# Kernel tuning notes

Measured on AMD Instinct MI355X. Metric: run time of the kernel, lower is better.

The kernel has to match this reference:

```python
import math
import jax, jax.numpy as jnp
import numpy as np

G = 128        # graphs per batch
N0 = 512       # nodes per graph
H = 256        # hidden size
E = 524288     # edges (avg degree 8), intra-graph
RATIO = 0.8


def setup_inputs() -> dict:
    key = jax.random.key(0)
    ks = jax.random.split(key, 16)
    # intra-graph edges: E//G edges per graph
    eg = jnp.arange(E, dtype=jnp.int32) // (E // G)
    src = eg * N0 + jax.random.randint(ks[0], (E,), 0, N0, dtype=jnp.int32)
    dst = eg * N0 + jax.random.randint(ks[1], (E,), 0, N0, dtype=jnp.int32)
    s = 1.0 / math.sqrt(H)
    return {
        "x": jax.random.normal(ks[2], (G * N0, H), jnp.float32),
        "edge_src": src,
        "edge_dst": dst,
        "W_in": jax.random.normal(ks[3], (H, H), jnp.float32) * s,
        "b_in": jnp.zeros((H,), jnp.float32),
        "W_h0": jax.random.normal(ks[4], (H, H), jnp.float32) * s,
        "b_h0": jnp.zeros((H,), jnp.float32),
        "W_h1": jax.random.normal(ks[5], (H, H), jnp.float32) * s,
        "b_h1": jnp.zeros((H,), jnp.float32),
        "p_in": jax.random.normal(ks[6], (H,), jnp.float32),
        "p_h0": jax.random.normal(ks[7], (H,), jnp.float32),
        "p_h1": jax.random.normal(ks[8], (H,), jnp.float32),
        "att_w": jax.random.normal(ks[9], (H,), jnp.float32) * s,
        "att_b": jnp.zeros((1,), jnp.float32),
    }


def gcn_conv(x, W, b, src, dst, emask, num_nodes):
    # PyG GCNConv: lin -> sym-normalized propagate (with self loops, weight 1) -> bias
    h = x @ W
    deg = jax.ops.segment_sum(emask, dst, num_segments=num_nodes) + 1.0  # +1 self loop
    dis = jax.lax.rsqrt(deg)
    coef = dis[src] * dis[dst] * emask                    # [E]
    agg = jax.ops.segment_sum(h[src] * coef[:, None], dst, num_segments=num_nodes)
    agg = agg + h * (dis * dis)[:, None]                  # self-loop message
    return agg + b


def topk_pool(x, p, src, dst, emask, n_cur):
    # PyG TopKPooling: score = tanh(x.p/|p|), keep top ceil(ratio*n) per graph,
    # x' = x[perm]*score[perm], edges filtered to kept nodes and remapped.
    k = int(math.ceil(RATIO * n_cur))
    score = jnp.tanh((x @ p) / jnp.linalg.norm(p))        # [G*n_cur]
    _, idx = jax.lax.top_k(score.reshape(G, n_cur), k)    # [G,k]
    perm = (idx + (jnp.arange(G, dtype=idx.dtype) * n_cur)[:, None]).reshape(-1)
    x_new = x[perm] * score[perm][:, None]                # [G*k,H]
    mapping = jnp.full((G * n_cur,), -1, jnp.int32).at[perm].set(
        jnp.arange(G * k, dtype=jnp.int32))
    ns, nd = mapping[src], mapping[dst]
    valid = (ns >= 0) & (nd >= 0) & (emask > 0)
    return (x_new, jnp.where(valid, ns, 0), jnp.where(valid, nd, 0),
            valid.astype(x.dtype), k)


def att_pool(x, att_w, att_b, k):
    # GlobalAttention: per-graph softmax gate, weighted sum
    gate = (x @ att_w + att_b[0]).reshape(G, k)
    att = jax.nn.softmax(gate, axis=1)
    return jnp.einsum('gk,gkh->gh', att, x.reshape(G, k, H))


def reference(x, edge_src, edge_dst, W_in, b_in, W_h0, b_h0, W_h1, b_h1,
              p_in, p_h0, p_h1, att_w, att_b):
    src, dst = edge_src, edge_dst
    emask = jnp.ones((E,), x.dtype)
    n_cur = N0
    h = jax.nn.relu(gcn_conv(x, W_in, b_in, src, dst, emask, G * n_cur))
    h, src, dst, emask, n_cur = topk_pool(h, p_in, src, dst, emask, n_cur)
    out = att_pool(h, att_w, att_b, n_cur)
    for (W, b, p) in ((W_h0, b_h0, p_h0), (W_h1, b_h1, p_h1)):
        h = jax.nn.relu(gcn_conv(h, W, b, src, dst, emask, G * n_cur))
        h, src, dst, emask, n_cur = topk_pool(h, p, src, dst, emask, n_cur)
        out = out + att_pool(h, att_w, att_b, n_cur)
    return out  # [G, H]
```

## Files before the change

### kernel.cpp

```cpp
#include <hip/hip_runtime.h>
#include <cmath>

#define G_ 128
#define N0_ 512
#define H_ 256
#define E_ 524288
#define NODES0 (G_*N0_)

typedef _Float16 v8h __attribute__((ext_vector_type(8)));
typedef _Float16 v4h __attribute__((ext_vector_type(4)));
typedef float v4f __attribute__((ext_vector_type(4)));

#define TSTRIDE 72
#define TILEHW (128*TSTRIDE)

__device__ __forceinline__ void async_copy16(void* lds, const void* g) {
  __builtin_amdgcn_global_load_lds(
      (const __attribute__((address_space(1))) void*)g,
      (__attribute__((address_space(3))) void*)lds, 16, 0, 0);
}

__device__ __forceinline__ float4 f4fma(float4 a, float s, float4 acc) {
  acc.x = fmaf(a.x, s, acc.x); acc.y = fmaf(a.y, s, acc.y);
  acc.z = fmaf(a.z, s, acc.z); acc.w = fmaf(a.w, s, acc.w);
  return acc;
}

__device__ __forceinline__ float block_reduce_sum(float v, volatile float* red) {
  #pragma unroll
  for (int off = 32; off > 0; off >>= 1) v += __shfl_down(v, off);
  int lane = threadIdx.x & 63, wid = threadIdx.x >> 6;
  __syncthreads();
  if (lane == 0) red[wid] = v;
  __syncthreads();
  return red[0] + red[1] + red[2] + red[3];
}

__global__ __launch_bounds__(256) void pnorm_kernel(const float* __restrict__ p0,
                                                    const float* __restrict__ p1,
                                                    const float* __restrict__ p2,
                                                    float* __restrict__ pinv) {
  __shared__ float red[4];
  const float* p = (blockIdx.x == 0) ? p0 : (blockIdx.x == 1 ? p1 : p2);
  float v = p[threadIdx.x];
  float s = block_reduce_sum(v * v, red);
  if (threadIdx.x == 0) pinv[blockIdx.x] = 1.0f / sqrtf(s);
}

__global__ void init_cum_kernel(int* __restrict__ cum, int* __restrict__ cnt, int n) {
  int v = blockIdx.x * 256 + threadIdx.x;
  if (v < n) { cum[v] = v; cnt[v] = 0; }
}

__global__ __launch_bounds__(256) void wconv_kernel(const float* __restrict__ W0,
                                                    const float* __restrict__ W1,
                                                    const float* __restrict__ W2,
                                                    _Float16* __restrict__ img) {
  int l = blockIdx.x >> 4;
  const float* W = (l == 0) ? W0 : (l == 1 ? W1 : W2);
  int bn = (blockIdx.x >> 3) & 1, kt = blockIdx.x & 7;
  int t = threadIdx.x;
  int n = t & 127, kh = t >> 7;
  int k0 = kt * 32 + kh * 16;
  _Float16* row = img + (size_t)l * 16 * TILEHW + ((size_t)(bn * 8 + kt) * 128 + n) * TSTRIDE;
  #pragma unroll
  for (int s = 0; s < 2; ++s) {
    v8h hv, lv;
    #pragma unroll
    for (int j = 0; j < 8; ++j) {
      float a = W[(size_t)(k0 + s * 8 + j) * 256 + bn * 128 + n];
      _Float16 h = (_Float16)a;
      hv[j] = h;
      lv[j] = (_Float16)(a - (float)h);
    }
    *(v8h*)&row[kh * 16 + s * 8] = hv;
    *(v8h*)&row[32 + kh * 16 + s * 8] = lv;
  }
}

__global__ __launch_bounds__(256) void gemm_f16x3_kernel(const float* __restrict__ A,
                                                         const _Float16* __restrict__ Wimg,
                                                         float* __restrict__ C) {
  __shared__ _Float16 As[TILEHW];
  __shared__ _Float16 Ws[TILEHW];
  const int tid = threadIdx.x;
  const int bm = blockIdx.x >> 1;
  const int bn = blockIdx.x & 1;
  const int lane = tid & 63, wid = tid >> 6;
  const int wm = wid >> 1, wn = wid & 1;
  const int l15 = lane & 15, kg = lane >> 4;

  v4f acc[4][4];
  #pragma unroll
  for (int i = 0; i < 4; ++i)
    #pragma unroll
    for (int j = 0; j < 4; ++j) acc[i][j] = (v4f){0.f, 0.f, 0.f, 0.f};

  int arow[4], acc4[4];
  const float* aptr[4];
  #pragma unroll
  for (int i = 0; i < 4; ++i) {
    int c = tid + 256 * i;
    arow[i] = c >> 3;
    acc4[i] = c & 7;
    aptr[i] = A + (size_t)(bm * 128 + arow[i]) * 256 + acc4[i] * 4;
  }
  const _Float16* wtile0 = Wimg + (size_t)bn * 8 * TILEHW;

  float4 pa[4];
  #pragma unroll
  for (int i = 0; i < 4; ++i) pa[i] = *(const float4*)(aptr[i] + 0);

  for (int kt = 0; kt < 8; ++kt) {
    {
      const _Float16* wt = wtile0 + (size_t)kt * TILEHW;
      for (int cb = wid; cb < 18; cb += 4)
        async_copy16(&Ws[cb * 512], wt + (size_t)cb * 512 + lane * 8);
    }
    #pragma unroll
    for (int i = 0; i < 4; ++i) {
      float av[4] = {pa[i].x, pa[i].y, pa[i].z, pa[i].w};
      v4h hv, lv;
      #pragma unroll
      for (int j = 0; j < 4; ++j) {
        _Float16 h = (_Float16)av[j];
        hv[j] = h;
        lv[j] = (_Float16)(av[j] - (float)h);
      }
      _Float16* dst = &As[arow[i] * TSTRIDE + acc4[i] * 4];
      *(v4h*)(dst) = hv;
      *(v4h*)(dst + 32) = lv;
    }
    __syncthreads();

    if (kt < 7) {
      #pragma unroll
      for (int i = 0; i < 4; ++i)
        pa[i] = *(const float4*)(aptr[i] + (kt + 1) * 32);
    }

    v8h ah[4], bh[4], al[4], bl[4];
    #pragma unroll
    for (int i = 0; i < 4; ++i)
      ah[i] = *(const v8h*)&As[(wm * 64 + i * 16 + l15) * TSTRIDE + kg * 8];
    #pragma unroll
    for (int j = 0; j < 4; ++j)
      bh[j] = *(const v8h*)&Ws[(wn * 64 + j * 16 + l15) * TSTRIDE + kg * 8];
    #pragma unroll
    for (int i = 0; i < 4; ++i)
      #pragma unroll
      for (int j = 0; j < 4; ++j)
        acc[i][j] = __builtin_amdgcn_mfma_f32_16x16x32_f16(ah[i], bh[j], acc[i][j], 0, 0, 0);
    #pragma unroll
    for (int i = 0; i < 4; ++i)
      al[i] = *(const v8h*)&As[(wm * 64 + i * 16 + l15) * TSTRIDE + 32 + kg * 8];
    #pragma unroll
    for (int i = 0; i < 4; ++i)
      #pragma unroll
      for (int j = 0; j < 4; ++j)
        acc[i][j] = __builtin_amdgcn_mfma_f32_16x16x32_f16(al[i], bh[j], acc[i][j], 0, 0, 0);
    #pragma unroll
    for (int j = 0; j < 4; ++j)
      bl[j] = *(const v8h*)&Ws[(wn * 64 + j * 16 + l15) * TSTRIDE + 32 + kg * 8];
    #pragma unroll
    for (int i = 0; i < 4; ++i)
      #pragma unroll
      for (int j = 0; j < 4; ++j)
        acc[i][j] = __builtin_amdgcn_mfma_f32_16x16x32_f16(ah[i], bl[j], acc[i][j], 0, 0, 0);
    __syncthreads();
  }

  #pragma unroll
  for (int i = 0; i < 4; ++i) {
    #pragma unroll
    for (int j = 0; j < 4; ++j) {
      #pragma unroll
      for (int r = 0; r < 4; ++r) {
        int row = bm * 128 + wm * 64 + i * 16 + kg * 4 + r;
        int col = bn * 128 + wn * 64 + j * 16 + l15;
        C[(size_t)row * 256 + col] = acc[i][j][r];
      }
    }
  }
}

__global__ void count_deg_kernel(const int* __restrict__ esrc, const int* __restrict__ edst,
                                 const int* __restrict__ cum, int* __restrict__ cnt) {
  int e = blockIdx.x * 256 + threadIdx.x;
  if (e >= E_) return;
  int ms = cum[esrc[e]], md = cum[edst[e]];
  if (ms >= 0 && md >= 0) atomicAdd(&cnt[md], 1);
}

__global__ __launch_bounds__(256) void scan1_kernel(const int* __restrict__ cnt,
                                                    int* __restrict__ row_start,
                                                    int* __restrict__ bsum,
                                                    float* __restrict__ dis,
                                                    int* __restrict__ cursor, int n) {
  __shared__ int sdata[256];
  int base = blockIdx.x * 1024;
  int t = threadIdx.x;
  int v[4]; int s = 0;
  #pragma unroll
  for (int i = 0; i < 4; ++i) {
    int idx = base + t * 4 + i;
    v[i] = (idx < n) ? cnt[idx] : 0;
    s += v[i];
    if (idx < n) {
      dis[idx] = 1.0f / sqrtf((float)v[i] + 1.0f);
      cursor[idx] = 0;
    }
  }
  sdata[t] = s;
  __syncthreads();
  for (int off = 1; off < 256; off <<= 1) {
    int x = (t >= off) ? sdata[t - off] : 0;
    __syncthreads();
    sdata[t] += x;
    __syncthreads();
  }
  int excl = sdata[t] - s;
  if (t == 255) bsum[blockIdx.x] = sdata[255];
  #pragma unroll
  for (int i = 0; i < 4; ++i) {
    int idx = base + t * 4 + i;
    if (idx < n) { row_start[idx] = excl; excl += v[i]; }
  }
}

__global__ __launch_bounds__(256) void scan2_kernel(int* __restrict__ bsum,
                                                    int* __restrict__ row_start, int nb, int n) {
  __shared__ int sdata[256];
  int t = threadIdx.x;
  int v = (t < nb) ? bsum[t] : 0;
  sdata[t] = v;
  __syncthreads();
  for (int off = 1; off < 256; off <<= 1) {
    int x = (t >= off) ? sdata[t - off] : 0;
    __syncthreads();
    sdata[t] += x;
    __syncthreads();
  }
  if (t < nb) bsum[t] = sdata[t] - v;
  if (t == 255) row_start[n] = sdata[255];
}

__global__ void fill_csr_kernel(const int* __restrict__ esrc, const int* __restrict__ edst,
                                const int* __restrict__ cum, const int* __restrict__ row_start,
                                const int* __restrict__ bsum,
                                int* __restrict__ cursor, const float* __restrict__ dis,
                                int* __restrict__ csr_src, float* __restrict__ csr_cf) {
  int e = blockIdx.x * 256 + threadIdx.x;
  if (e >= E_) return;
  int ms = cum[esrc[e]], md = cum[edst[e]];
  if (ms < 0 || md < 0) return;
  int pos = atomicAdd(&cursor[md], 1);
  int j = row_start[md] + bsum[md >> 10] + pos;
  csr_src[j] = ms;
  csr_cf[j] = dis[ms] * dis[md];
}

__global__ __launch_bounds__(256) void agg_score_kernel(
    const float4* __restrict__ hlin4, const float* __restrict__ dis,
    const float4* __restrict__ bias4,
    const int* __restrict__ row_start, const int* __restrict__ bsum,
    const int* __restrict__ csr_src,
    const float* __restrict__ csr_cf, const float4* __restrict__ p4,
    const float* __restrict__ pinvp,
    float4* __restrict__ hout4, float* __restrict__ score,
    int* __restrict__ cnt, int n, int q) {
  int blk = (blockIdx.x & 7) * q + (blockIdx.x >> 3);
  int wave = threadIdx.x >> 6, lane = threadIdx.x & 63;
  int v = blk * 4 + wave;
  float dv = dis[v];
  float self = dv * dv;
  float4 h = hlin4[(size_t)v * 64 + lane];
  float4 acc = make_float4(h.x * self, h.y * self, h.z * self, h.w * self);
  int rs = row_start[v] + bsum[v >> 10];
  int v1 = v + 1;
  int re = row_start[v1] + ((v1 < n) ? bsum[v1 >> 10] : 0);
  if (lane == 0) cnt[v] = 0;
  int j = rs;
  for (; j + 8 <= re; j += 8) {
    int s[8]; float c[8]; float4 hh[8];
    #pragma unroll
    for (int u = 0; u < 8; ++u) { s[u] = csr_src[j + u]; c[u] = csr_cf[j + u]; }
    #pragma unroll
    for (int u = 0; u < 8; ++u) hh[u] = hlin4[(size_t)s[u] * 64 + lane];
    #pragma unroll
    for (int u = 0; u < 8; ++u) acc = f4fma(hh[u], c[u], acc);
  }
  if (j + 4 <= re) {
    int s[4]; float c[4]; float4 hh[4];
    #pragma unroll
    for (int u = 0; u < 4; ++u) { s[u] = csr_src[j + u]; c[u] = csr_cf[j + u]; }
    #pragma unroll
    for (int u = 0; u < 4; ++u) hh[u] = hlin4[(size_t)s[u] * 64 + lane];
    #pragma unroll
    for (int u = 0; u < 4; ++u) acc = f4fma(hh[u], c[u], acc);
    j += 4;
  }
  for (; j < re; ++j) {
    acc = f4fma(hlin4[(size_t)csr_src[j] * 64 + lane], csr_cf[j], acc);
  }
  float4 b = bias4[lane];
  acc.x = fmaxf(acc.x + b.x, 0.0f); acc.y = fmaxf(acc.y + b.y, 0.0f);
  acc.z = fmaxf(acc.z + b.z, 0.0f); acc.w = fmaxf(acc.w + b.w, 0.0f);
  hout4[(size_t)v * 64 + lane] = acc;
  float4 pv = p4[lane];
  float s = acc.x * pv.x + acc.y * pv.y + acc.z * pv.z + acc.w * pv.w;
  #pragma unroll
  for (int off = 32; off > 0; off >>= 1) s += __shfl_down(s, off);
  if (lane == 0) score[v] = tanhf(s * pinvp[0]);
}

__global__ __launch_bounds__(256) void topk_kernel(const float* __restrict__ score, int n, int k,
                                                   int* __restrict__ cum, int* __restrict__ perm) {
  __shared__ float key[512];
  __shared__ int kid[512];
  __shared__ int newmap[512];
  int g = blockIdx.x, t = threadIdx.x;
  for (int i = t; i < 512; i += 256) {
    key[i] = (i < n) ? score[(size_t)g * n + i] : -INFINITY;
    kid[i] = i;
    if (i < n) newmap[i] = -1;
  }
  __syncthreads();
  for (int kk = 2; kk <= 512; kk <<= 1) {
    for (int j = kk >> 1; j > 0; j >>= 1) {
      #pragma unroll
      for (int half = 0; half < 2; ++half) {
        int i = t + half * 256;
        int ixj = i ^ j;
        if (ixj > i) {
          float ka = key[i]; int ia = kid[i];
          float kb = key[ixj]; int ib = kid[ixj];
          bool b_first = (kb > ka) || (kb == ka && ib < ia);
          bool sw = ((i & kk) == 0) ? b_first : !b_first;
          if (sw) { key[i] = kb; kid[i] = ib; key[ixj] = ka; kid[ixj] = ia; }
        }
      }
      __syncthreads();
    }
  }
  for (int i = t; i < k; i += 256) {
    int local = kid[i];
    perm[g * k + i] = g * n + local;
    newmap[local] = g * k + i;
  }
  __syncthreads();
  #pragma unroll
  for (int u = 0; u < N0_ / 256; ++u) {
    int v = g * N0_ + u * 256 + t;
    int c = cum[v];
    if (c >= 0) cum[v] = newmap[c - g * n];
  }
}

__global__ __launch_bounds__(512) void pool_kernel(
    const float4* __restrict__ h4, const float* __restrict__ score,
    const int* __restrict__ perm,
    const float4* __restrict__ attw4, const float* __restrict__ attb,
    float4* __restrict__ xnew4, float* __restrict__ out, int k, int add) {
  __shared__ float wmax[8], wsum[8];
  __shared__ float4 waccs[8][64];
  int g = blockIdx.x, t = threadIdx.x;
  int wave = t >> 6, lane = t & 63;
  float4 aw = attw4[lane];
  float ab = attb[0];

  float m = -INFINITY, ssum = 0.0f;
  float4 acc = make_float4(0.f, 0.f, 0.f, 0.f);
  for (int i = wave; i < k; i += 8) {
    int s = perm[g * k + i];
    float sc = score[s];
    float4 hv = h4[(size_t)s * 64 + lane];
    float4 val = make_float4(hv.x * sc, hv.y * sc, hv.z * sc, hv.w * sc);
    xnew4[((size_t)g * k + i) * 64 + lane] = val;
    float gd = val.x * aw.x + val.y * aw.y + val.z * aw.z + val.w * aw.w;
    #pragma unroll
    for (int off = 32; off > 0; off >>= 1) gd += __shfl_xor(gd, off);
    float gi = gd + ab;
    float mnew = fmaxf(m, gi);
    float f = __expf(m - mnew);
    float e = __expf(gi - mnew);
    acc.x = acc.x * f + val.x * e; acc.y = acc.y * f + val.y * e;
    acc.z = acc.z * f + val.z * e; acc.w = acc.w * f + val.w * e;
    ssum = ssum * f + e;
    m = mnew;
  }
  if (lane == 0) { wmax[wave] = m; wsum[wave] = ssum; }
  waccs[wave][lane] = acc;
  __syncthreads();
  if (wave == 0) {
    float mstar = wmax[0];
    #pragma unroll
    for (int w = 1; w < 8; ++w) mstar = fmaxf(mstar, wmax[w]);
    float stot = 0.0f;
    float4 a = make_float4(0.f, 0.f, 0.f, 0.f);
    #pragma unroll
    for (int w = 0; w < 8; ++w) {
      float sc = __expf(wmax[w] - mstar);
      stot += wsum[w] * sc;
      float4 wa = waccs[w][lane];
      a.x += wa.x * sc; a.y += wa.y * sc; a.z += wa.z * sc; a.w += wa.w * sc;
    }
    float inv = 1.0f / stot;
    a.x *= inv; a.y *= inv; a.z *= inv; a.w *= inv;
    float4* o4 = (float4*)out + (size_t)g * 64 + lane;
    if (add) {
      float4 prev = *o4;
      a.x += prev.x; a.y += prev.y; a.z += prev.z; a.w += prev.w;
    }
    *o4 = a;
  }
}

extern "C" void kernel_launch(void* const* d_in, const int* in_sizes, int n_in,
                              void* d_out, int out_size, void* d_ws, size_t ws_size,
                              hipStream_t stream) {
  const float* x    = (const float*)d_in[0];
  const int*   esrc = (const int*)d_in[1];
  const int*   edst = (const int*)d_in[2];
  const float* Wl[3] = {(const float*)d_in[3], (const float*)d_in[5], (const float*)d_in[7]};
  const float* bl[3] = {(const float*)d_in[4], (const float*)d_in[6], (const float*)d_in[8]};
  const float* pl[3] = {(const float*)d_in[9], (const float*)d_in[10], (const float*)d_in[11]};
  const float* attw = (const float*)d_in[12];
  const float* attb = (const float*)d_in[13];
  float* out = (float*)d_out;

  char* w = (char*)d_ws;
  auto carve = [&](size_t bytes) { char* p = w; w += (bytes + 255) & ~(size_t)255; return p; };
  float* bufA    = (float*)carve((size_t)NODES0 * H_ * 4);
  float* bufB    = (float*)carve((size_t)NODES0 * H_ * 4);
  int*   csr_src = (int*)  carve((size_t)E_ * 4);
  float* csr_cf  = (float*)carve((size_t)E_ * 4);
  int*   cnt     = (int*)  carve((size_t)NODES0 * 4);
  int*   row_st  = (int*)  carve((size_t)(NODES0 + 1) * 4);
  int*   cursor  = (int*)  carve((size_t)NODES0 * 4);
  float* dis     = (float*)carve((size_t)NODES0 * 4);
  float* score   = (float*)carve((size_t)NODES0 * 4);
  int*   cum_map = (int*)  carve((size_t)NODES0 * 4);
  int*   perm    = (int*)  carve((size_t)NODES0 * 4);
  int*   bsum    = (int*)  carve(256 * 4);
  float* pinv    = (float*)carve(16);
  _Float16* Wimg = (_Float16*)carve((size_t)3 * 16 * TILEHW * 2);
  (void)ws_size; (void)in_sizes; (void)n_in; (void)out_size;

  pnorm_kernel<<<3, 256, 0, stream>>>(pl[0], pl[1], pl[2], pinv);
  init_cum_kernel<<<NODES0 / 256, 256, 0, stream>>>(cum_map, cnt, NODES0);
  wconv_kernel<<<48, 256, 0, stream>>>(Wl[0], Wl[1], Wl[2], Wimg);

  int n_cur = N0_;
  const float* xin = x;
  for (int l = 0; l < 3; ++l) {
    int nodes = G_ * n_cur;
    float* hlin = (l & 1) ? bufB : bufA;
    float* hbuf = (l & 1) ? bufA : bufB;
    float* xnew = hlin;

    gemm_f16x3_kernel<<<(nodes / 128) * 2, 256, 0, stream>>>(
        xin, Wimg + (size_t)l * 16 * TILEHW, hlin);

    count_deg_kernel<<<E_ / 256, 256, 0, stream>>>(esrc, edst, cum_map, cnt);
    int nb = (nodes + 1023) / 1024;
    scan1_kernel<<<nb, 256, 0, stream>>>(cnt, row_st, bsum, dis, cursor, nodes);
    scan2_kernel<<<1, 256, 0, stream>>>(bsum, row_st, nb, nodes);
    fill_csr_kernel<<<E_ / 256, 256, 0, stream>>>(esrc, edst, cum_map, row_st, bsum, cursor,
                                                  dis, csr_src, csr_cf);

    int agg_blocks = nodes / 4;
    agg_score_kernel<<<agg_blocks, 256, 0, stream>>>(
        (const float4*)hlin, dis, (const float4*)bl[l], row_st, bsum, csr_src, csr_cf,
        (const float4*)pl[l], pinv + l, (float4*)hbuf, score, cnt, nodes, agg_blocks / 8);

    int kk = (int)std::ceil(0.8 * (double)n_cur);
    topk_kernel<<<G_, 256, 0, stream>>>(score, n_cur, kk, cum_map, perm);

    pool_kernel<<<G_, 512, 0, stream>>>(
        (const float4*)hbuf, score, perm, (const float4*)attw, attb,
        (float4*)xnew, out, kk, l > 0 ? 1 : 0);

    n_cur = kk;
    xin = xnew;
  }
}
```

Measured before the change: 443.3 us.

## Build CSR once over original nodes and fuse pooled gather into GEMM

Builds the CSR once on the original node ids and tracks an orig_of mapping through pooling. Later layers filter neighbours through cum_map inside the aggregation, and a small deg_kernel recomputes degrees from the original CSR. The per-layer count/scan/fill passes go away. The pooled feature write (x[perm]*score) is also removed and folded into the GEMM's A-load through perm indexing and scaling. Together these save a full-size write/read of features each layer, at the cost of gathered, non-contiguous GEMM A loads and traversing filtered-out edges during aggregation.

```diff
diff --git a/kernel.cpp b/kernel.cpp
--- a/kernel.cpp
+++ b/kernel.cpp
@@ -47,9 +47,10 @@
   if (threadIdx.x == 0) pinv[blockIdx.x] = 1.0f / sqrtf(s);
 }
 
-__global__ void init_cum_kernel(int* __restrict__ cum, int* __restrict__ cnt, int n) {
+__global__ void init_kernel(int* __restrict__ cum, int* __restrict__ orig_of,
+                            int* __restrict__ cnt, int n) {
   int v = blockIdx.x * 256 + threadIdx.x;
-  if (v < n) { cum[v] = v; cnt[v] = 0; }
+  if (v < n) { cum[v] = v; orig_of[v] = v; cnt[v] = 0; }
 }
 
 __global__ __launch_bounds__(256) void wconv_kernel(const float* __restrict__ W0,
@@ -78,7 +79,91 @@
   }
 }
 
+__global__ void count0_kernel(const int* __restrict__ edst, int* __restrict__ cnt) {
+  int e = blockIdx.x * 256 + threadIdx.x;
+  if (e < E_) atomicAdd(&cnt[edst[e]], 1);
+}
+
+__global__ __launch_bounds__(256) void scan1_kernel(const int* __restrict__ cnt,
+                                                    int* __restrict__ row0,
+                                                    int* __restrict__ bsum,
+                                                    float* __restrict__ dis,
+                                                    int* __restrict__ cursor, int n) {
+  __shared__ int sdata[256];
+  int base = blockIdx.x * 1024;
+  int t = threadIdx.x;
+  int v[4]; int s = 0;
+  #pragma unroll
+  for (int i = 0; i < 4; ++i) {
+    int idx = base + t * 4 + i;
+    v[i] = (idx < n) ? cnt[idx] : 0;
+    s += v[i];
+    if (idx < n) {
+      dis[idx] = 1.0f / sqrtf((float)v[i] + 1.0f);
+      cursor[idx] = 0;
+    }
+  }
+  sdata[t] = s;
+  __syncthreads();
+  for (int off = 1; off < 256; off <<= 1) {
+    int x = (t >= off) ? sdata[t - off] : 0;
+    __syncthreads();
+    sdata[t] += x;
+    __syncthreads();
+  }
+  int excl = sdata[t] - s;
+  if (t == 255) bsum[blockIdx.x] = sdata[255];
+  #pragma unroll
+  for (int i = 0; i < 4; ++i) {
+    int idx = base + t * 4 + i;
+    if (idx < n) { row0[idx] = excl; excl += v[i]; }
+  }
+}
+
+__global__ __launch_bounds__(256) void scan2_kernel(int* __restrict__ bsum,
+                                                    int* __restrict__ row0, int nb, int n) {
+  __shared__ int sdata[256];
+  int t = threadIdx.x;
+  int v = (t < nb) ? bsum[t] : 0;
+  sdata[t] = v;
+  __syncthreads();
+  for (int off = 1; off < 256; off <<= 1) {
+    int x = (t >= off) ? sdata[t - off] : 0;
+    __syncthreads();
+    sdata[t] += x;
+    __syncthreads();
+  }
+  if (t < nb) bsum[t] = sdata[t] - v;
+  if (t == 255) row0[n] = sdata[255];
+}
+
+__global__ void fill0_kernel(const int* __restrict__ esrc, const int* __restrict__ edst,
+                             const int* __restrict__ row0, const int* __restrict__ bsum,
+                             int* __restrict__ cursor, int* __restrict__ csr0) {
+  int e = blockIdx.x * 256 + threadIdx.x;
+  if (e >= E_) return;
+  int d = edst[e];
+  int pos = atomicAdd(&cursor[d], 1);
+  csr0[row0[d] + bsum[d >> 10] + pos] = esrc[e];
+}
+
+__global__ void deg_kernel(const int* __restrict__ orig_of, const int* __restrict__ row0,
+                           const int* __restrict__ bsum, const int* __restrict__ csr0,
+                           const int* __restrict__ cum, float* __restrict__ dis, int nodes) {
+  int v = blockIdx.x * 256 + threadIdx.x;
+  if (v >= nodes) return;
+  int o = orig_of[v];
+  int rs = row0[o] + bsum[o >> 10];
+  int o1 = o + 1;
+  int re = row0[o1] + ((o1 < NODES0) ? bsum[o1 >> 10] : 0);
+  int c = 0;
+  for (int j = rs; j < re; ++j) c += (cum[csr0[j]] >= 0) ? 1 : 0;
+  dis[v] = rsqrtf((float)c + 1.0f);
+}
+
 __global__ __launch_bounds__(256) void gemm_f16x3_kernel(const float* __restrict__ A,
+                                                         const int* __restrict__ perm,
+                                                         const float* __restrict__ score,
                                                          const _Float16* __restrict__ Wimg,
                                                          float* __restrict__ C) {
   __shared__ _Float16 As[TILEHW];
@@ -98,12 +183,16 @@
 
   int arow[4], acc4[4];
   const float* aptr[4];
+  float ascale[4];
   #pragma unroll
   for (int i = 0; i < 4; ++i) {
     int c = tid + 256 * i;
     arow[i] = c >> 3;
     acc4[i] = c & 7;
-    aptr[i] = A + (size_t)(bm * 128 + arow[i]) * 256 + acc4[i] * 4;
+    int R = bm * 128 + arow[i];
+    int pr = perm ? perm[R] : R;
+    ascale[i] = perm ? score[pr] : 1.0f;
+    aptr[i] = A + (size_t)pr * 256 + acc4[i] * 4;
   }
   const _Float16* wtile0 = Wimg + (size_t)bn * 8 * TILEHW;
 
@@ -119,7 +208,8 @@
     }
     #pragma unroll
     for (int i = 0; i < 4; ++i) {
-      float av[4] = {pa[i].x, pa[i].y, pa[i].z, pa[i].w};
+      float av[4] = {pa[i].x * ascale[i], pa[i].y * ascale[i],
+                     pa[i].z * ascale[i], pa[i].w * ascale[i]};
       v4h hv, lv;
       #pragma unroll
       for (int j = 0; j < 4; ++j) {
@@ -184,91 +274,14 @@
   }
 }
 
-__global__ void count_deg_kernel(const int* __restrict__ esrc, const int* __restrict__ edst,
-                                 const int* __restrict__ cum, int* __restrict__ cnt) {
-  int e = blockIdx.x * 256 + threadIdx.x;
-  if (e >= E_) return;
-  int ms = cum[esrc[e]], md = cum[edst[e]];
-  if (ms >= 0 && md >= 0) atomicAdd(&cnt[md], 1);
-}
-
-__global__ __launch_bounds__(256) void scan1_kernel(const int* __restrict__ cnt,
-                                                    int* __restrict__ row_start,
-                                                    int* __restrict__ bsum,
-                                                    float* __restrict__ dis,
-                                                    int* __restrict__ cursor, int n) {
-  __shared__ int sdata[256];
-  int base = blockIdx.x * 1024;
-  int t = threadIdx.x;
-  int v[4]; int s = 0;
-  #pragma unroll
-  for (int i = 0; i < 4; ++i) {
-    int idx = base + t * 4 + i;
-    v[i] = (idx < n) ? cnt[idx] : 0;
-    s += v[i];
-    if (idx < n) {
-      dis[idx] = 1.0f / sqrtf((float)v[i] + 1.0f);
-      cursor[idx] = 0;
-    }
-  }
-  sdata[t] = s;
-  __syncthreads();
-  for (int off = 1; off < 256; off <<= 1) {
-    int x = (t >= off) ? sdata[t - off] : 0;
-    __syncthreads();
-    sdata[t] += x;
-    __syncthreads();
-  }
-  int excl = sdata[t] - s;
-  if (t == 255) bsum[blockIdx.x] = sdata[255];
-  #pragma unroll
-  for (int i = 0; i < 4; ++i) {
-    int idx = base + t * 4 + i;
-    if (idx < n) { row_start[idx] = excl; excl += v[i]; }
-  }
-}
-
-__global__ __launch_bounds__(256) void scan2_kernel(int* __restrict__ bsum,
-                                                    int* __restrict__ row_start, int nb, int n) {
-  __shared__ int sdata[256];
-  int t = threadIdx.x;
-  int v = (t < nb) ? bsum[t] : 0;
-  sdata[t] = v;
-  __syncthreads();
-  for (int off = 1; off < 256; off <<= 1) {
-    int x = (t >= off) ? sdata[t - off] : 0;
-    __syncthreads();
-    sdata[t] += x;
-    __syncthreads();
-  }
-  if (t < nb) bsum[t] = sdata[t] - v;
-  if (t == 255) row_start[n] = sdata[255];
-}
-
-__global__ void fill_csr_kernel(const int* __restrict__ esrc, const int* __restrict__ edst,
-                                const int* __restrict__ cum, const int* __restrict__ row_start,
-                                const int* __restrict__ bsum,
-                                int* __restrict__ cursor, const float* __restrict__ dis,
-                                int* __restrict__ csr_src, float* __restrict__ csr_cf) {
-  int e = blockIdx.x * 256 + threadIdx.x;
-  if (e >= E_) return;
-  int ms = cum[esrc[e]], md = cum[edst[e]];
-  if (ms < 0 || md < 0) return;
-  int pos = atomicAdd(&cursor[md], 1);
-  int j = row_start[md] + bsum[md >> 10] + pos;
-  csr_src[j] = ms;
-  csr_cf[j] = dis[ms] * dis[md];
-}
-
 __global__ __launch_bounds__(256) void agg_score_kernel(
     const float4* __restrict__ hlin4, const float* __restrict__ dis,
     const float4* __restrict__ bias4,
-    const int* __restrict__ row_start, const int* __restrict__ bsum,
-    const int* __restrict__ csr_src,
-    const float* __restrict__ csr_cf, const float4* __restrict__ p4,
-    const float* __restrict__ pinvp,
-    float4* __restrict__ hout4, float* __restrict__ score,
-    int* __restrict__ cnt, int n, int q) {
+    const int* __restrict__ orig_of, const int* __restrict__ row0,
+    const int* __restrict__ bsum, const int* __restrict__ csr0,
+    const int* __restrict__ cum,
+    const float4* __restrict__ p4, const float* __restrict__ pinvp,
+    float4* __restrict__ hout4, float* __restrict__ score, int q) {
   int blk = (blockIdx.x & 7) * q + (blockIdx.x >> 3);
   int wave = threadIdx.x >> 6, lane = threadIdx.x & 63;
   int v = blk * 4 + wave;
@@ -276,32 +289,30 @@
   float self = dv * dv;
   float4 h = hlin4[(size_t)v * 64 + lane];
   float4 acc = make_float4(h.x * self, h.y * self, h.z * self, h.w * self);
-  int rs = row_start[v] + bsum[v >> 10];
-  int v1 = v + 1;
-  int re = row_start[v1] + ((v1 < n) ? bsum[v1 >> 10] : 0);
-  if (lane == 0) cnt[v] = 0;
+  int o = orig_of[v];
+  int rs = row0[o] + bsum[o >> 10];
+  int o1 = o + 1;
+  int re = row0[o1] + ((o1 < NODES0) ? bsum[o1 >> 10] : 0);
   int j = rs;
-  for (; j + 8 <= re; j += 8) {
-    int s[8]; float c[8]; float4 hh[8];
-    #pragma unroll
-    for (int u = 0; u < 8; ++u) { s[u] = csr_src[j + u]; c[u] = csr_cf[j + u]; }
-    #pragma unroll
-    for (int u = 0; u < 8; ++u) hh[u] = hlin4[(size_t)s[u] * 64 + lane];
-    #pragma unroll
-    for (int u = 0; u < 8; ++u) acc = f4fma(hh[u], c[u], acc);
-  }
-  if (j + 4 <= re) {
-    int s[4]; float c[4]; float4 hh[4];
-    #pragma unroll
-    for (int u = 0; u < 4; ++u) { s[u] = csr_src[j + u]; c[u] = csr_cf[j + u]; }
-    #pragma unroll
-    for (int u = 0; u < 4; ++u) hh[u] = hlin4[(size_t)s[u] * 64 + lane];
-    #pragma unroll
-    for (int u = 0; u < 4; ++u) acc = f4fma(hh[u], c[u], acc);
-    j += 4;
-  }
-  for (; j < re; ++j) {
-    acc = f4fma(hlin4[(size_t)csr_src[j] * 64 + lane], csr_cf[j], acc);
+  while (j < re) {
+    int mrem = re - j;
+    int c[8]; float cf[8];
+    #pragma unroll
+    for (int u = 0; u < 8; ++u) {
+      if (u < mrem) {
+        int cc = cum[csr0[j + u]];
+        c[u] = cc;
+        cf[u] = (cc >= 0) ? dis[cc] * dv : 0.0f;
+      } else c[u] = -1;
+    }
+    float4 hh[8];
+    #pragma unroll
+    for (int u = 0; u < 8; ++u)
+      if (c[u] >= 0) hh[u] = hlin4[(size_t)c[u] * 64 + lane];
+    #pragma unroll
+    for (int u = 0; u < 8; ++u)
+      if (c[u] >= 0) acc = f4fma(hh[u], cf[u], acc);
+    j += (mrem < 8) ? mrem : 8;
   }
   float4 b = bias4[lane];
   acc.x = fmaxf(acc.x + b.x, 0.0f); acc.y = fmaxf(acc.y + b.y, 0.0f);
@@ -315,7 +326,10 @@
 }
 
 __global__ __launch_bounds__(256) void topk_kernel(const float* __restrict__ score, int n, int k,
-                                                   int* __restrict__ cum, int* __restrict__ perm) {
+                                                   int* __restrict__ cum,
+                                                   const int* __restrict__ orig_prev,
+                                                   int* __restrict__ orig_new,
+                                                   int* __restrict__ perm) {
   __shared__ float key[512];
   __shared__ int kid[512];
   __shared__ int newmap[512];
@@ -347,6 +361,7 @@
     int local = kid[i];
     perm[g * k + i] = g * n + local;
     newmap[local] = g * k + i;
+    orig_new[g * k + i] = orig_prev[g * n + local];
   }
   __syncthreads();
   #pragma unroll
@@ -361,7 +376,7 @@
     const float4* __restrict__ h4, const float* __restrict__ score,
     const int* __restrict__ perm,
     const float4* __restrict__ attw4, const float* __restrict__ attb,
-    float4* __restrict__ xnew4, float* __restrict__ out, int k, int add) {
+    float* __restrict__ out, int k, int add) {
   __shared__ float wmax[8], wsum[8];
   __shared__ float4 waccs[8][64];
   int g = blockIdx.x, t = threadIdx.x;
@@ -376,7 +391,6 @@
     float sc = score[s];
     float4 hv = h4[(size_t)s * 64 + lane];
     float4 val = make_float4(hv.x * sc, hv.y * sc, hv.z * sc, hv.w * sc);
-    xnew4[((size_t)g * k + i) * 64 + lane] = val;
     float gd = val.x * aw.x + val.y * aw.y + val.z * aw.z + val.w * aw.w;
     #pragma unroll
     for (int off = 32; off > 0; off >>= 1) gd += __shfl_xor(gd, off);
@@ -433,14 +447,15 @@
   auto carve = [&](size_t bytes) { char* p = w; w += (bytes + 255) & ~(size_t)255; return p; };
   float* bufA    = (float*)carve((size_t)NODES0 * H_ * 4);
   float* bufB    = (float*)carve((size_t)NODES0 * H_ * 4);
-  int*   csr_src = (int*)  carve((size_t)E_ * 4);
-  float* csr_cf  = (float*)carve((size_t)E_ * 4);
+  int*   csr0    = (int*)  carve((size_t)E_ * 4);
   int*   cnt     = (int*)  carve((size_t)NODES0 * 4);
-  int*   row_st  = (int*)  carve((size_t)(NODES0 + 1) * 4);
+  int*   row0    = (int*)  carve((size_t)(NODES0 + 1) * 4);
   int*   cursor  = (int*)  carve((size_t)NODES0 * 4);
   float* dis     = (float*)carve((size_t)NODES0 * 4);
   float* score   = (float*)carve((size_t)NODES0 * 4);
   int*   cum_map = (int*)  carve((size_t)NODES0 * 4);
+  int*   origA   = (int*)  carve((size_t)NODES0 * 4);
+  int*   origB   = (int*)  carve((size_t)NODES0 * 4);
   int*   perm    = (int*)  carve((size_t)NODES0 * 4);
   int*   bsum    = (int*)  carve(256 * 4);
   float* pinv    = (float*)carve(16);
@@ -448,40 +463,42 @@
   (void)ws_size; (void)in_sizes; (void)n_in; (void)out_size;
 
   pnorm_kernel<<<3, 256, 0, stream>>>(pl[0], pl[1], pl[2], pinv);
-  init_cum_kernel<<<NODES0 / 256, 256, 0, stream>>>(cum_map, cnt, NODES0);
+  init_kernel<<<NODES0 / 256, 256, 0, stream>>>(cum_map, origA, cnt, NODES0);
   wconv_kernel<<<48, 256, 0, stream>>>(Wl[0], Wl[1], Wl[2], Wimg);
 
+  count0_kernel<<<E_ / 256, 256, 0, stream>>>(edst, cnt);
+  int nb0 = (NODES0 + 1023) / 1024;
+  scan1_kernel<<<nb0, 256, 0, stream>>>(cnt, row0, bsum, dis, cursor, NODES0);
+  scan2_kernel<<<1, 256, 0, stream>>>(bsum, row0, nb0, NODES0);
+  fill0_kernel<<<E_ / 256, 256, 0, stream>>>(esrc, edst, row0, bsum, cursor, csr0);
+
   int n_cur = N0_;
-  const float* xin = x;
+  int* origs[2] = {origA, origB};
   for (int l = 0; l < 3; ++l) {
     int nodes = G_ * n_cur;
-    float* hlin = (l & 1) ? bufB : bufA;
-    float* hbuf = (l & 1) ? bufA : bufB;
-    float* xnew = hlin;
+    int* orig_cur = origs[l & 1];
+    int* orig_nxt = origs[(l & 1) ^ 1];
+
+    if (l > 0) {
+      deg_kernel<<<(nodes + 255) / 256, 256, 0, stream>>>(orig_cur, row0, bsum, csr0,
+                                                          cum_map, dis, nodes);
+    }
 
     gemm_f16x3_kernel<<<(nodes / 128) * 2, 256, 0, stream>>>(
-        xin, Wimg + (size_t)l * 16 * TILEHW, hlin);
-
-    count_deg_kernel<<<E_ / 256, 256, 0, stream>>>(esrc, edst, cum_map, cnt);
-    int nb = (nodes + 1023) / 1024;
-    scan1_kernel<<<nb, 256, 0, stream>>>(cnt, row_st, bsum, dis, cursor, nodes);
-    scan2_kernel<<<1, 256, 0, stream>>>(bsum, row_st, nb, nodes);
-    fill_csr_kernel<<<E_ / 256, 256, 0, stream>>>(esrc, edst, cum_map, row_st, bsum, cursor,
-                                                  dis, csr_src, csr_cf);
+        (l == 0) ? x : bufB, (l == 0) ? nullptr : perm, score,
+        Wimg + (size_t)l * 16 * TILEHW, bufA);
 
     int agg_blocks = nodes / 4;
     agg_score_kernel<<<agg_blocks, 256, 0, stream>>>(
-        (const float4*)hlin, dis, (const float4*)bl[l], row_st, bsum, csr_src, csr_cf,
-        (const float4*)pl[l], pinv + l, (float4*)hbuf, score, cnt, nodes, agg_blocks / 8);
+        (const float4*)bufA, dis, (const float4*)bl[l], orig_cur, row0, bsum, csr0,
+        cum_map, (const float4*)pl[l], pinv + l, (float4*)bufB, score, agg_blocks / 8);
 
     int kk = (int)std::ceil(0.8 * (double)n_cur);
-    topk_kernel<<<G_, 256, 0, stream>>>(score, n_cur, kk, cum_map, perm);
+    topk_kernel<<<G_, 256, 0, stream>>>(score, n_cur, kk, cum_map, orig_cur, orig_nxt, perm);
 
     pool_kernel<<<G_, 512, 0, stream>>>(
-        (const float4*)hbuf, score, perm, (const float4*)attw, attb,
-        (float4*)xnew, out, kk, l > 0 ? 1 : 0);
+        (const float4*)bufB, score, perm, (const float4*)attw, attb, out, kk, l > 0 ? 1 : 0);
 
     n_cur = kk;
-    xin = xnew;
-  }
-}
+  }
+}
```

Result: slower. 466.1 us (+5.1%).
